# Optimization experiments

Hardware: AMD Instinct MI355X
Metric: run time of the kernel (lower is better)

The kernel has to match this reference:

```python
import jax, jax.numpy as jnp
import numpy as np

H = 6  # num_heads
D = 384  # embedding_dim


def _rot(seg, coord):
    # seg: [BN, H, T, L], coord: [BN, T]; rotate interleaved even/odd pairs
    L = seg.shape[-1]
    pairs = max(L // 2, 1)
    inv_freq = 1.0 / (10000.0 ** (jnp.arange(pairs, dtype=seg.dtype) / pairs))
    ang = coord[..., None] * inv_freq          # [BN, T, pairs]
    cos = jnp.cos(ang)[:, None]                # [BN, 1, T, pairs]
    sin = jnp.sin(ang)[:, None]
    even, odd = seg[..., 0::2], seg[..., 1::2]
    re = even * cos - odd * sin
    ro = even * sin + odd * cos
    return jnp.stack((re, ro), axis=-1).reshape(seg.shape)


def _apply_rope3(t, pos, chunk):
    # t: [BN, H, T, Hd], pos: [BN, T, 3]; three axis chunks, tail untouched
    parts, s = [], 0
    for i in range(3):
        parts.append(_rot(t[..., s:s + chunk], pos[..., i]))
        s += chunk
    parts.append(t[..., s:])
    return jnp.concatenate(parts, axis=-1)


def setup_inputs() -> dict:
    key = jax.random.key(0)
    ks = jax.random.split(key, 10)
    B, N, T = 8, 64, 128
    scale = 1.0 / np.sqrt(D)
    return {
        "padded_batches": jax.random.normal(ks[0], (B, N, T, D), jnp.float32),
        "sum_token": jax.random.normal(ks[1], (B, N, 1, D), jnp.float32),
        "positions_3d": jax.random.uniform(ks[2], (B, N, T, 3), jnp.float32),
        "Wq": jax.random.normal(ks[3], (D, D), jnp.float32) * scale,
        "bq": jax.random.normal(ks[4], (D,), jnp.float32) * scale,
        "Wk": jax.random.normal(ks[5], (D, D), jnp.float32) * scale,
        "bk": jax.random.normal(ks[6], (D,), jnp.float32) * scale,
        "Wv": jax.random.normal(ks[7], (D, D), jnp.float32) * scale,
        "bv": jax.random.normal(ks[8], (D,), jnp.float32) * scale,
        "masks": jax.random.randint(ks[9], (B, N, T), 0, 2, jnp.int32),
    }


def reference(padded_batches, sum_token, positions_3d, Wq, bq, Wk, bk, Wv, bv, masks):
    B, N, T, Dm = padded_batches.shape
    Hd = Dm // H
    chunk = Hd // 6 * 2

    # masked mean-pool summary token (summary_mode='avg')
    w = masks[..., None].astype(padded_batches.dtype)          # [B,N,T,1]
    denom = jnp.clip(w.sum(axis=-2, keepdims=True), 1e-6, None)
    summary = (padded_batches * w).sum(axis=-2, keepdims=True) / denom  # [B,N,1,D]

    q = (padded_batches @ Wq + bq).reshape(B * N, T, H, Hd).transpose(0, 2, 1, 3)  # [BN,H,T,Hd]
    k = (summary @ Wk + bk).reshape(B * N, 1, H, Hd).transpose(0, 2, 1, 3)         # [BN,H,1,Hd]
    v = (summary @ Wv + bv).reshape(B * N, 1, H, Hd).transpose(0, 2, 1, 3)

    # 3-axis RoPE on q (token positions) and k (pooled positions)
    pos_summary = (positions_3d * w).sum(axis=-2, keepdims=True) / denom  # [B,N,1,3]
    pos_q = positions_3d.reshape(B * N, T, 3)
    pos_k = pos_summary.reshape(B * N, 1, 3)
    q = _apply_rope3(q, pos_q, chunk)
    k = _apply_rope3(k, pos_k, chunk)

    # SDPA with T queries vs 1 key
    scores = jnp.einsum('bhtd,bhkd->bhtk', q, k) / np.float32(np.sqrt(Hd))  # [BN,H,T,1]
    mask_add = jnp.where(masks.reshape(B * N, 1, T, 1) == 0,
                         jnp.finfo(jnp.float32).min, 0.0)
    attn_w = jax.nn.softmax(scores + mask_add, axis=-1)
    attn = jnp.einsum('bhtk,bhkd->bhtd', attn_w, v)  # [BN,H,T,Hd]

    out = attn.transpose(0, 2, 1, 3).reshape(B, N, T, Dm) + padded_batches
    return out
```

## Files before the change

### kernel.cpp

```cpp
#include <hip/hip_runtime.h>


#define DM 384
#define TT 128
#define C4 96
#define NBLK 256
#define NR  8
#define RPT 16

typedef float f32x4 __attribute__((ext_vector_type(4)));

__device__ __forceinline__ void nt_store4(float4* p, const float4 v) {
    __builtin_nontemporal_store(*(const f32x4*)&v, (f32x4*)p);
}

__global__ __launch_bounds__(768) void fused_pair(
    const float* __restrict__ padded,
    const int*   __restrict__ masks,
    const float* __restrict__ Wv,
    const float* __restrict__ bv,
    float*       __restrict__ out)
{
    const int bn0 = blockIdx.x << 1;
    const int t = threadIdx.x;
    const int c = t % C4;
    const int r = t / C4;

    __shared__ float  w_sh[2][TT];
    __shared__ float4 part_sh[2][NR][C4];
    __shared__ float  summ[2][DM];

    int m = 0;
    if (t < 2 * TT) m = masks[bn0 * TT + t];

    const float4* __restrict__ p0 = (const float4*)padded + (size_t)bn0 * TT * C4;
    const float4* __restrict__ p1 = p0 + TT * C4;

    float4 x0[RPT], x1[RPT];
    #pragma unroll
    for (int i = 0; i < RPT; ++i) x0[i] = p0[(r + i * NR) * C4 + c];
    #pragma unroll
    for (int i = 0; i < RPT; ++i) x1[i] = p1[(r + i * NR) * C4 + c];

    if (t < TT)          w_sh[0][t]      = (float)m;
    else if (t < 2 * TT) w_sh[1][t - TT] = (float)m;
    __syncthreads();

    float4 acc0 = make_float4(0.f, 0.f, 0.f, 0.f);
    float4 acc1 = make_float4(0.f, 0.f, 0.f, 0.f);
    #pragma unroll
    for (int i = 0; i < RPT; ++i) {
        const float w = w_sh[0][r + i * NR];
        acc0.x += x0[i].x * w; acc0.y += x0[i].y * w;
        acc0.z += x0[i].z * w; acc0.w += x0[i].w * w;
    }
    #pragma unroll
    for (int i = 0; i < RPT; ++i) {
        const float w = w_sh[1][r + i * NR];
        acc1.x += x1[i].x * w; acc1.y += x1[i].y * w;
        acc1.z += x1[i].z * w; acc1.w += x1[i].w * w;
    }
    part_sh[0][r][c] = acc0;
    part_sh[1][r][c] = acc1;

    #pragma unroll
    for (int i = 0; i < RPT; ++i) {
        asm volatile("" : "+v"(x0[i].x), "+v"(x0[i].y), "+v"(x0[i].z), "+v"(x0[i].w));
        asm volatile("" : "+v"(x1[i].x), "+v"(x1[i].y), "+v"(x1[i].z), "+v"(x1[i].w));
    }
    __syncthreads();

    if (t < 2 * C4) {
        const int s  = (t >= C4);
        const int cc = t - s * C4;
        float d0 = 0.f, d1 = 0.f, d2 = 0.f, d3 = 0.f;
        #pragma unroll
        for (int i = 0; i < 32; ++i) {
            d0 += w_sh[s][i];      d1 += w_sh[s][32 + i];
            d2 += w_sh[s][64 + i]; d3 += w_sh[s][96 + i];
        }
        const float inv = 1.0f / fmaxf((d0 + d1) + (d2 + d3), 1e-6f);

        float4 sm = part_sh[s][0][cc];
        #pragma unroll
        for (int g = 1; g < NR; ++g) {
            const float4 p = part_sh[s][g][cc];
            sm.x += p.x; sm.y += p.y; sm.z += p.z; sm.w += p.w;
        }
        sm.x *= inv; sm.y *= inv; sm.z *= inv; sm.w *= inv;
        ((float4*)summ[s])[cc] = sm;
    }
    __syncthreads();

    float4 a0 = make_float4(0.f, 0.f, 0.f, 0.f);
    float4 a1 = make_float4(0.f, 0.f, 0.f, 0.f);
    const float4* __restrict__ wv4 = (const float4*)Wv;
    const int e0 = r * (DM / NR);
    #pragma unroll 8
    for (int i = 0; i < DM / NR; ++i) {
        const int   e  = e0 + i;
        const float s0 = summ[0][e];
        const float s1 = summ[1][e];
        const float4 w = wv4[(size_t)e * C4 + c];
        a0.x += s0 * w.x; a0.y += s0 * w.y; a0.z += s0 * w.z; a0.w += s0 * w.w;
        a1.x += s1 * w.x; a1.y += s1 * w.y; a1.z += s1 * w.z; a1.w += s1 * w.w;
    }
    part_sh[0][r][c] = a0;
    part_sh[1][r][c] = a1;
    __syncthreads();

    float4 v0 = ((const float4*)bv)[c];
    float4 v1 = v0;
    #pragma unroll
    for (int g = 0; g < NR; ++g) {
        const float4 q0 = part_sh[0][g][c];
        const float4 q1 = part_sh[1][g][c];
        v0.x += q0.x; v0.y += q0.y; v0.z += q0.z; v0.w += q0.w;
        v1.x += q1.x; v1.y += q1.y; v1.z += q1.z; v1.w += q1.w;
    }

    float4* __restrict__ o0 = (float4*)out + (size_t)bn0 * TT * C4;
    float4* __restrict__ o1 = o0 + TT * C4;
    #pragma unroll
    for (int i = 0; i < RPT; ++i) {
        float4 y = x0[i];
        y.x += v0.x; y.y += v0.y; y.z += v0.z; y.w += v0.w;
        nt_store4(&o0[(r + i * NR) * C4 + c], y);
    }
    #pragma unroll
    for (int i = 0; i < RPT; ++i) {
        float4 y = x1[i];
        y.x += v1.x; y.y += v1.y; y.z += v1.z; y.w += v1.w;
        nt_store4(&o1[(r + i * NR) * C4 + c], y);
    }
}

extern "C" void kernel_launch(void* const* d_in, const int* in_sizes, int n_in,
                              void* d_out, int out_size, void* d_ws, size_t ws_size,
                              hipStream_t stream) {
    const float* padded = (const float*)d_in[0];
    const float* Wv     = (const float*)d_in[7];
    const float* bv     = (const float*)d_in[8];
    const int*   masks  = (const int*)d_in[9];
    float* out = (float*)d_out;

    fused_pair<<<NBLK, 768, 0, stream>>>(padded, masks, Wv, bv, out);
}
```

Baseline: 219.1 us.

## Re-read input tiles instead of holding them in registers, raise occupancy

The kernel no longer keeps all 32 float4 input rows per thread in registers across the pooling, projection and output phases. It streams them during the masked sum, using four independent accumulators, and loads them again from global memory (expected to hit cache) when writing the output. A launch-bounds hint asks for more resident blocks per CU. This trades a second read of the 50MB input for lower register pressure and more occupancy. The reload may miss in L2 or MALL and double HBM traffic.

```diff
diff --git a/kernel.cpp b/kernel.cpp
--- a/kernel.cpp
+++ b/kernel.cpp
@@ -14,7 +14,7 @@
     __builtin_nontemporal_store(*(const f32x4*)&v, (f32x4*)p);
 }
 
-__global__ __launch_bounds__(768) void fused_pair(
+__global__ __launch_bounds__(768, 4) void fused_seqpair(
     const float* __restrict__ padded,
     const int*   __restrict__ masks,
     const float* __restrict__ Wv,
@@ -22,51 +22,60 @@
     float*       __restrict__ out)
 {
     const int bn0 = blockIdx.x << 1;
-    const int t = threadIdx.x;
-    const int c = t % C4;
-    const int r = t / C4;
+    const int t   = threadIdx.x;
+    const int c   = t % C4;
+    const int r   = t / C4;
 
     __shared__ float  w_sh[2][TT];
-    __shared__ float4 part_sh[2][NR][C4];
+    __shared__ float4 partA[NR][C4];
+    __shared__ float4 partB[NR][C4];
     __shared__ float  summ[2][DM];
 
-    int m = 0;
-    if (t < 2 * TT) m = masks[bn0 * TT + t];
+    if (t < 2 * TT) w_sh[t >> 7][t & (TT - 1)] = (float)masks[bn0 * TT + t];
 
-    const float4* __restrict__ p0 = (const float4*)padded + (size_t)bn0 * TT * C4;
-    const float4* __restrict__ p1 = p0 + TT * C4;
+    const float4* __restrict__ pA = (const float4*)padded + (size_t)bn0 * TT * C4;
+    const float4* __restrict__ pB = pA + TT * C4;
 
-    float4 x0[RPT], x1[RPT];
-    #pragma unroll
-    for (int i = 0; i < RPT; ++i) x0[i] = p0[(r + i * NR) * C4 + c];
-    #pragma unroll
-    for (int i = 0; i < RPT; ++i) x1[i] = p1[(r + i * NR) * C4 + c];
-
-    if (t < TT)          w_sh[0][t]      = (float)m;
-    else if (t < 2 * TT) w_sh[1][t - TT] = (float)m;
     __syncthreads();
 
-    float4 acc0 = make_float4(0.f, 0.f, 0.f, 0.f);
-    float4 acc1 = make_float4(0.f, 0.f, 0.f, 0.f);
-    #pragma unroll
-    for (int i = 0; i < RPT; ++i) {
-        const float w = w_sh[0][r + i * NR];
-        acc0.x += x0[i].x * w; acc0.y += x0[i].y * w;
-        acc0.z += x0[i].z * w; acc0.w += x0[i].w * w;
+    {
+        float4 a0 = make_float4(0.f,0.f,0.f,0.f), a1 = a0, a2 = a0, a3 = a0;
+        #pragma unroll
+        for (int i = 0; i < 4; ++i) {
+            const int  r0 = r + (4*i    ) * NR, r1 = r + (4*i + 1) * NR;
+            const int  r2 = r + (4*i + 2) * NR, r3 = r + (4*i + 3) * NR;
+            const float w0 = w_sh[0][r0], w1 = w_sh[0][r1];
+            const float w2 = w_sh[0][r2], w3 = w_sh[0][r3];
+            const float4 x0 = pA[r0 * C4 + c], x1 = pA[r1 * C4 + c];
+            const float4 x2 = pA[r2 * C4 + c], x3 = pA[r3 * C4 + c];
+            a0.x += x0.x*w0; a0.y += x0.y*w0; a0.z += x0.z*w0; a0.w += x0.w*w0;
+            a1.x += x1.x*w1; a1.y += x1.y*w1; a1.z += x1.z*w1; a1.w += x1.w*w1;
+            a2.x += x2.x*w2; a2.y += x2.y*w2; a2.z += x2.z*w2; a2.w += x2.w*w2;
+            a3.x += x3.x*w3; a3.y += x3.y*w3; a3.z += x3.z*w3; a3.w += x3.w*w3;
+        }
+        a0.x += a1.x + a2.x + a3.x; a0.y += a1.y + a2.y + a3.y;
+        a0.z += a1.z + a2.z + a3.z; a0.w += a1.w + a2.w + a3.w;
+        partA[r][c] = a0;
     }
-    #pragma unroll
-    for (int i = 0; i < RPT; ++i) {
-        const float w = w_sh[1][r + i * NR];
-        acc1.x += x1[i].x * w; acc1.y += x1[i].y * w;
-        acc1.z += x1[i].z * w; acc1.w += x1[i].w * w;
-    }
-    part_sh[0][r][c] = acc0;
-    part_sh[1][r][c] = acc1;
 
-    #pragma unroll
-    for (int i = 0; i < RPT; ++i) {
-        asm volatile("" : "+v"(x0[i].x), "+v"(x0[i].y), "+v"(x0[i].z), "+v"(x0[i].w));
-        asm volatile("" : "+v"(x1[i].x), "+v"(x1[i].y), "+v"(x1[i].z), "+v"(x1[i].w));
+    {
+        float4 a0 = make_float4(0.f,0.f,0.f,0.f), a1 = a0, a2 = a0, a3 = a0;
+        #pragma unroll
+        for (int i = 0; i < 4; ++i) {
+            const int  r0 = r + (4*i    ) * NR, r1 = r + (4*i + 1) * NR;
+            const int  r2 = r + (4*i + 2) * NR, r3 = r + (4*i + 3) * NR;
+            const float w0 = w_sh[1][r0], w1 = w_sh[1][r1];
+            const float w2 = w_sh[1][r2], w3 = w_sh[1][r3];
+            const float4 x0 = pB[r0 * C4 + c], x1 = pB[r1 * C4 + c];
+            const float4 x2 = pB[r2 * C4 + c], x3 = pB[r3 * C4 + c];
+            a0.x += x0.x*w0; a0.y += x0.y*w0; a0.z += x0.z*w0; a0.w += x0.w*w0;
+            a1.x += x1.x*w1; a1.y += x1.y*w1; a1.z += x1.z*w1; a1.w += x1.w*w1;
+            a2.x += x2.x*w2; a2.y += x2.y*w2; a2.z += x2.z*w2; a2.w += x2.w*w2;
+            a3.x += x3.x*w3; a3.y += x3.y*w3; a3.z += x3.z*w3; a3.w += x3.w*w3;
+        }
+        a0.x += a1.x + a2.x + a3.x; a0.y += a1.y + a2.y + a3.y;
+        a0.z += a1.z + a2.z + a3.z; a0.w += a1.w + a2.w + a3.w;
+        partB[r][c] = a0;
     }
     __syncthreads();
 
@@ -81,10 +90,11 @@
         }
         const float inv = 1.0f / fmaxf((d0 + d1) + (d2 + d3), 1e-6f);
 
-        float4 sm = part_sh[s][0][cc];
+        const float4* part = s ? &partB[0][0] : &partA[0][0];
+        float4 sm = part[cc];
         #pragma unroll
         for (int g = 1; g < NR; ++g) {
-            const float4 p = part_sh[s][g][cc];
+            const float4 p = part[g * C4 + cc];
             sm.x += p.x; sm.y += p.y; sm.z += p.z; sm.w += p.w;
         }
         sm.x *= inv; sm.y *= inv; sm.z *= inv; sm.w *= inv;
@@ -92,46 +102,50 @@
     }
     __syncthreads();
 
-    float4 a0 = make_float4(0.f, 0.f, 0.f, 0.f);
-    float4 a1 = make_float4(0.f, 0.f, 0.f, 0.f);
-    const float4* __restrict__ wv4 = (const float4*)Wv;
-    const int e0 = r * (DM / NR);
-    #pragma unroll 8
-    for (int i = 0; i < DM / NR; ++i) {
-        const int   e  = e0 + i;
-        const float s0 = summ[0][e];
-        const float s1 = summ[1][e];
-        const float4 w = wv4[(size_t)e * C4 + c];
-        a0.x += s0 * w.x; a0.y += s0 * w.y; a0.z += s0 * w.z; a0.w += s0 * w.w;
-        a1.x += s1 * w.x; a1.y += s1 * w.y; a1.z += s1 * w.z; a1.w += s1 * w.w;
+    {
+        float4 aA = make_float4(0.f,0.f,0.f,0.f);
+        float4 aB = make_float4(0.f,0.f,0.f,0.f);
+        const float4* __restrict__ wv4 = (const float4*)Wv;
+        const int e0 = r * (DM / NR);
+        #pragma unroll 8
+        for (int i = 0; i < DM / NR; ++i) {
+            const int   e  = e0 + i;
+            const float sA = summ[0][e];
+            const float sB = summ[1][e];
+            const float4 w = wv4[(size_t)e * C4 + c];
+            aA.x += sA*w.x; aA.y += sA*w.y; aA.z += sA*w.z; aA.w += sA*w.w;
+            aB.x += sB*w.x; aB.y += sB*w.y; aB.z += sB*w.z; aB.w += sB*w.w;
+        }
+        partA[r][c] = aA;
+        partB[r][c] = aB;
     }
-    part_sh[0][r][c] = a0;
-    part_sh[1][r][c] = a1;
     __syncthreads();
 
-    float4 v0 = ((const float4*)bv)[c];
-    float4 v1 = v0;
+    const float4 b = ((const float4*)bv)[c];
+    float4 vA = b, vB = b;
     #pragma unroll
     for (int g = 0; g < NR; ++g) {
-        const float4 q0 = part_sh[0][g][c];
-        const float4 q1 = part_sh[1][g][c];
-        v0.x += q0.x; v0.y += q0.y; v0.z += q0.z; v0.w += q0.w;
-        v1.x += q1.x; v1.y += q1.y; v1.z += q1.z; v1.w += q1.w;
+        const float4 qA = partA[g][c];
+        const float4 qB = partB[g][c];
+        vA.x += qA.x; vA.y += qA.y; vA.z += qA.z; vA.w += qA.w;
+        vB.x += qB.x; vB.y += qB.y; vB.z += qB.z; vB.w += qB.w;
     }
 
-    float4* __restrict__ o0 = (float4*)out + (size_t)bn0 * TT * C4;
-    float4* __restrict__ o1 = o0 + TT * C4;
+    float4* __restrict__ oA = (float4*)out + (size_t)bn0 * TT * C4;
+    float4* __restrict__ oB = oA + TT * C4;
     #pragma unroll
     for (int i = 0; i < RPT; ++i) {
-        float4 y = x0[i];
-        y.x += v0.x; y.y += v0.y; y.z += v0.z; y.w += v0.w;
-        nt_store4(&o0[(r + i * NR) * C4 + c], y);
+        const int idx = (r + i * NR) * C4 + c;
+        float4 x = pA[idx];
+        x.x += vA.x; x.y += vA.y; x.z += vA.z; x.w += vA.w;
+        nt_store4(&oA[idx], x);
     }
     #pragma unroll
     for (int i = 0; i < RPT; ++i) {
-        float4 y = x1[i];
-        y.x += v1.x; y.y += v1.y; y.z += v1.z; y.w += v1.w;
-        nt_store4(&o1[(r + i * NR) * C4 + c], y);
+        const int idx = (r + i * NR) * C4 + c;
+        float4 x = pB[idx];
+        x.x += vB.x; x.y += vB.y; x.z += vB.z; x.w += vB.w;
+        nt_store4(&oB[idx], x);
     }
 }
 
@@ -144,5 +158,5 @@
     const int*   masks  = (const int*)d_in[9];
     float* out = (float*)d_out;
 
-    fused_pair<<<NBLK, 768, 0, stream>>>(padded, masks, Wv, bv, out);
+    fused_seqpair<<<NBLK, 768, 0, stream>>>(padded, masks, Wv, bv, out);
 }
```

Result: faster. 213.5 us (-2.6%).
